# Optimization experiments

Hardware: AMD Instinct MI355X
Metric: run time of the kernel (lower is better)

## Reference

```python
import jax, jax.numpy as jnp
import numpy as np
import math

H = 12   # num_attention_heads
DH = 64  # attention_head_size
D = H * DH  # hidden_size = 768


def _split_heads(x):
    # [b, s, D] -> [b, H, s, DH]
    b, s, _ = x.shape
    return x.reshape(b, s, H, DH).transpose(0, 2, 1, 3)


def setup_inputs() -> dict:
    key = jax.random.key(0)
    ks = jax.random.split(key, 8)
    B, S, G, NUM_CTX = 32, 512, 16, 8
    real_b = B // NUM_CTX
    inp = {
        "hidden_states": jax.random.normal(ks[0], (B, S, D), dtype=jnp.float32),
        "attention_mask": jnp.zeros((B, 1, 1, S), dtype=jnp.float32),
        "global_tokens_embed": jax.random.normal(ks[1], (real_b, G, D), dtype=jnp.float32),
        "Wq": jax.random.normal(ks[2], (D, D), dtype=jnp.float32) * 0.02,
        "bq": jnp.zeros((D,), dtype=jnp.float32),
        "Wk": jax.random.normal(ks[3], (D, D), dtype=jnp.float32) * 0.02,
        "bk": jnp.zeros((D,), dtype=jnp.float32),
        "Wv": jax.random.normal(ks[4], (D, D), dtype=jnp.float32) * 0.02,
        "bv": jnp.zeros((D,), dtype=jnp.float32),
        "num_ctx": 8,
    }
    return inp


def reference(hidden_states, attention_mask, global_tokens_embed,
              Wq, bq, Wk, bk, Wv, bv, num_ctx):
    B, S, _ = hidden_states.shape
    real_b = B // num_ctx
    G = global_tokens_embed.shape[1]
    scale = 1.0 / math.sqrt(DH)

    # Q/K/V projections for packed contexts
    q = _split_heads(hidden_states @ Wq + bq)   # [B,H,S,DH]
    k = _split_heads(hidden_states @ Wk + bk)
    v = _split_heads(hidden_states @ Wv + bv)

    # Global token projections
    gq = _split_heads(global_tokens_embed @ Wq + bq)  # [real_b,H,G,DH]
    gk = _split_heads(global_tokens_embed @ Wk + bk)
    gv = _split_heads(global_tokens_embed @ Wv + bv)

    # ---- Global-token cross attention over all contexts of each real batch ----
    # [B,H,S,DH] -> [real_b, H, num_ctx*S, DH]
    full_k = k.transpose(0, 2, 1, 3).reshape(real_b, num_ctx * S, H, DH).transpose(0, 2, 1, 3)
    full_v = v.transpose(0, 2, 1, 3).reshape(real_b, num_ctx * S, H, DH).transpose(0, 2, 1, 3)
    full_k = jnp.concatenate([gk, full_k], axis=2)  # [real_b,H,G+num_ctx*S,DH]
    full_v = jnp.concatenate([gv, full_v], axis=2)

    g_scores = jnp.einsum('bhgd,bhkd->bhgk', gq, full_k) * scale
    g_mask = attention_mask.reshape(real_b, num_ctx * S)[:, None, None, :]
    g_mask = jnp.concatenate([jnp.zeros((real_b, 1, 1, G), g_mask.dtype), g_mask], axis=3)
    g_scores = g_scores + g_mask
    g_probs = jax.nn.softmax(g_scores, axis=-1)
    g_ctx = jnp.einsum('bhgk,bhkd->bhgd', g_probs, full_v)
    g_ctx = g_ctx.transpose(0, 2, 1, 3).reshape(real_b, G, D)  # [real_b,G,D]

    # ---- Local attention: each context attends to its own tokens + global tokens ----
    gk_rep = jnp.broadcast_to(gk[:, None], (real_b, num_ctx, H, G, DH)).reshape(B, H, G, DH)
    gv_rep = jnp.broadcast_to(gv[:, None], (real_b, num_ctx, H, G, DH)).reshape(B, H, G, DH)
    k2 = jnp.concatenate([gk_rep, k], axis=2)  # [B,H,G+S,DH]
    v2 = jnp.concatenate([gv_rep, v], axis=2)
    mask2 = jnp.concatenate([jnp.zeros((B, 1, 1, G), attention_mask.dtype), attention_mask], axis=3)

    scores = jnp.einsum('bhqd,bhkd->bhqk', q, k2) * scale + mask2  # [B,H,S,G+S]
    probs = jax.nn.softmax(scores, axis=-1)
    ctx = jnp.einsum('bhqk,bhkd->bhqd', probs, v2)
    ctx = ctx.transpose(0, 2, 1, 3).reshape(B, S, D)  # [B,S,D]

    return ctx, g_ctx
```

## Files before the change

kernel.cpp:

```cpp
#include <hip/hip_runtime.h>
#include <hip/hip_bf16.h>
#include <stdint.h>

#define NH 12
#define DHD 64
#define DM 768
#define BB 32
#define SS 512
#define GG 16
#define NCTX 8
#define RBATCH 4
#define OUTG_OFF ((size_t)BB * SS * DM)

#define XROWS 16512
#define NALL 2304
#define NX8 (XROWS * DM / 8)
#define NB8 (NALL / 8)
#define NM8 (BB * SS / 8)

#define LOG2E 1.4426950408889634f
#define QSCALE 0.18033688011112042f

typedef __bf16 bf16x8 __attribute__((ext_vector_type(8)));
typedef float f32x4 __attribute__((ext_vector_type(4)));
typedef float f32x16 __attribute__((ext_vector_type(16)));

__device__ __forceinline__ float b2f(unsigned short u) {
    union { unsigned int i; float f; } x;
    x.i = ((unsigned int)u) << 16;
    return x.f;
}
__device__ __forceinline__ unsigned short f2b(float f) {
    __hip_bfloat16 h = __float2bfloat16(f);
    return *reinterpret_cast<unsigned short*>(&h);
}
__device__ __forceinline__ unsigned int pk2(float a, float b) {
    return ((unsigned int)f2b(b) << 16) | (unsigned int)f2b(a);
}
__device__ __forceinline__ float ex2(float x) {
    return __builtin_amdgcn_exp2f(x);
}
__device__ __forceinline__ float ldv(const void* p, size_t i, int isf32) {
    return isf32 ? ((const float*)p)[i] : b2f(((const unsigned short*)p)[i]);
}
__device__ __forceinline__ void stv(void* p, size_t i, int isf32, float v) {
    if (isf32) ((float*)p)[i] = v;
    else       ((unsigned short*)p)[i] = f2b(v);
}
__device__ __forceinline__ void async_cp16(const unsigned short* g, unsigned short* l) {
    __builtin_amdgcn_global_load_lds(
        (const __attribute__((address_space(1))) unsigned int*)g,
        (__attribute__((address_space(3))) unsigned int*)l, 16, 0, 0);
}

__device__ __forceinline__ void vt_pair_store(unsigned int* Vt32, int vr, int scc,
                                              uint4 a, uint4 b, int ldq) {
    const unsigned int* au = (const unsigned int*)&a;
    const unsigned int* bu = (const unsigned int*)&b;
    #pragma unroll
    for (int i = 0; i < 4; i++) {
        const int d0 = scc + 2 * i;
        const int swz = ((vr >> 3) ^ ((d0 >> 3) & 7));
        const int i32 = d0 * ldq + (swz << 2) + ((vr & 7) >> 1);
        Vt32[i32]       = __builtin_amdgcn_perm(bu[i], au[i], 0x05040100u);
        Vt32[i32 + ldq] = __builtin_amdgcn_perm(bu[i], au[i], 0x07060302u);
    }
}

__global__ __launch_bounds__(256) void detect_dtype(
    const unsigned short* __restrict__ Wq, int* __restrict__ flag)
{
    __shared__ int hi, zz;
    if (threadIdx.x == 0) { hi = 0; zz = 0; }
    __syncthreads();
    int lh = 0, lz = 0;
    for (int i = threadIdx.x; i < 4096; i += 256) {
        unsigned short u = Wq[2 * i];
        if (((u >> 7) & 0xFF) >= 130) lh++;
        if (u == 0) lz++;
    }
    atomicAdd(&hi, lh);
    atomicAdd(&zz, lz);
    __syncthreads();
    if (threadIdx.x == 0) *flag = (hi > 512 || zz > 3500) ? 1 : 0;
}

__global__ __launch_bounds__(256) void cvt_x(
    const void* __restrict__ hs, const void* __restrict__ gte,
    const void* __restrict__ bq, const void* __restrict__ bk,
    const void* __restrict__ bv, const void* __restrict__ mask,
    const int* __restrict__ flag,
    unsigned short* __restrict__ Xb, unsigned short* __restrict__ b_all,
    unsigned short* __restrict__ wmask)
{
    const int e = blockIdx.x * 256 + threadIdx.x;
    const int isf32 = *flag;
    if (e < NX8) {
        const int base = e * 8;
        const int row = base / DM, col = base % DM;
        unsigned short o8[8];
        if (row < 16384) {
            if (isf32) {
                float4 a = ((const float4*)hs)[e * 2];
                float4 c = ((const float4*)hs)[e * 2 + 1];
                o8[0]=f2b(a.x); o8[1]=f2b(a.y); o8[2]=f2b(a.z); o8[3]=f2b(a.w);
                o8[4]=f2b(c.x); o8[5]=f2b(c.y); o8[6]=f2b(c.z); o8[7]=f2b(c.w);
            } else {
                *(uint4*)o8 = ((const uint4*)hs)[e];
            }
        } else if (row < 16448) {
            size_t soff = (size_t)(row - 16384) * DM + col;
            #pragma unroll
            for (int i = 0; i < 8; i++) o8[i] = f2b(ldv(gte, soff + i, isf32));
        } else {
            #pragma unroll
            for (int i = 0; i < 8; i++) o8[i] = 0;
        }
        *(uint4*)&Xb[base] = *(const uint4*)o8;
    } else if (e < NX8 + NB8) {
        const int i0 = (e - NX8) * 8;
        #pragma unroll
        for (int i = 0; i < 8; i++) {
            int ng = i0 + i;
            int z = ng / DM;
            const void* src = (z == 0) ? bq : (z == 1) ? bk : bv;
            b_all[ng] = f2b(ldv(src, ng % DM, isf32));
        }
    } else if (e < NX8 + NB8 + NM8) {
        const int i0 = (e - NX8 - NB8) * 8;
        #pragma unroll
        for (int i = 0; i < 8; i++)
            wmask[i0 + i] = f2b(ldv(mask, i0 + i, isf32) * LOG2E);
    }
}

__global__ __launch_bounds__(256) void cvt_w(
    const void* __restrict__ Wq, const void* __restrict__ Wk,
    const void* __restrict__ Wv, const int* __restrict__ flag,
    unsigned short* __restrict__ Wt)
{
    __shared__ float T[64][65];
    const int kt = blockIdx.x;
    const int ngt = blockIdx.y;
    const int z = ngt / 12, nt = ngt % 12;
    const int tid = threadIdx.x;
    const int isf32 = *flag;
    const void* W = (z == 0) ? Wq : (z == 1) ? Wk : Wv;

    for (int jj = 0; jj < 16; jj++) {
        int el = tid + jj * 256;
        int r = el >> 6, c = el & 63;
        T[r][c] = ldv(W, (size_t)(kt * 64 + r) * DM + nt * 64 + c, isf32);
    }
    __syncthreads();
    for (int jj = 0; jj < 16; jj++) {
        int el = tid + jj * 256;
        int rn = el >> 6, ck = el & 63;
        Wt[(size_t)(z * DM + nt * 64 + rn) * DM + kt * 64 + ck] = f2b(T[ck][rn]);
    }
}

#define QKV_NWG (129 * 18)
__global__ __launch_bounds__(256) void qkv_gemm(
    const unsigned short* __restrict__ Xb,
    const unsigned short* __restrict__ Wt,
    const unsigned short* __restrict__ b_all,
    unsigned short* __restrict__ q, unsigned short* __restrict__ kk_,
    unsigned short* __restrict__ v,
    unsigned short* __restrict__ gq, unsigned short* __restrict__ gk,
    unsigned short* __restrict__ gv)
{
    __shared__ __align__(16) unsigned short As[2][128 * 32];
    __shared__ __align__(16) unsigned short Bs[2][128 * 32];

    const int orig = blockIdx.x;
    const int q8 = QKV_NWG >> 3, r8 = QKV_NWG & 7;
    const int xcd = orig & 7, lin = orig >> 3;
    const int swz = (xcd < r8 ? xcd * (q8 + 1) : r8 * (q8 + 1) + (xcd - r8) * q8) + lin;
    const int mt = swz / 18, nt = swz - mt * 18;

    const int tid = threadIdx.x;
    const int wave = tid >> 6, lane = tid & 63;
    const int quad = lane >> 4, l16 = lane & 15;
    const int wm = wave & 1, wn = wave >> 1;
    const int z = nt / 6;
    unsigned short* YL = (z == 0) ? q : (z == 1) ? kk_ : v;
    unsigned short* YG = (z == 0) ? gq : (z == 1) ? gk : gv;
    const float qsc = (z == 0) ? QSCALE : 1.0f;

    const int sr = tid >> 2, sc = (tid & 3) * 8;

    const unsigned short* Arow0 = &Xb[(size_t)(mt * 128 + sr) * DM + sc];
    const unsigned short* Arow1 = Arow0 + (size_t)64 * DM;
    const unsigned short* Brow0 = &Wt[(size_t)(nt * 128 + sr) * DM + sc];
    const unsigned short* Brow1 = Brow0 + (size_t)64 * DM;

    f32x4 acc[4][4];
    #pragma unroll
    for (int i = 0; i < 4; i++)
        for (int j = 0; j < 4; j++)
            for (int r = 0; r < 4; r++) acc[i][j][r] = 0.f;

    async_cp16(Arow0, &As[0][wave * 512]);
    async_cp16(Arow1, &As[0][2048 + wave * 512]);
    async_cp16(Brow0, &Bs[0][wave * 512]);
    async_cp16(Brow1, &Bs[0][2048 + wave * 512]);
    __syncthreads();

    int cur = 0;
    for (int t = 0; t < 24; t++) {
        if (t < 23) {
            const int kn = (t + 1) * 32;
            async_cp16(Arow0 + kn, &As[cur ^ 1][wave * 512]);
            async_cp16(Arow1 + kn, &As[cur ^ 1][2048 + wave * 512]);
            async_cp16(Brow0 + kn, &Bs[cur ^ 1][wave * 512]);
            async_cp16(Brow1 + kn, &Bs[cur ^ 1][2048 + wave * 512]);
        }

        bf16x8 af[4], bf[4];
        #pragma unroll
        for (int ib = 0; ib < 4; ib++)
            af[ib] = *(const bf16x8*)&As[cur][(wm * 64 + ib * 16 + l16) * 32 + quad * 8];
        #pragma unroll
        for (int jb = 0; jb < 4; jb++)
            bf[jb] = *(const bf16x8*)&Bs[cur][(wn * 64 + jb * 16 + l16) * 32 + quad * 8];
        #pragma unroll
        for (int ib = 0; ib < 4; ib++)
            #pragma unroll
            for (int jb = 0; jb < 4; jb++)
                acc[ib][jb] = __builtin_amdgcn_mfma_f32_16x16x32_bf16(
                    bf[jb], af[ib], acc[ib][jb], 0, 0, 0);

        if (t < 23) __syncthreads();
        cur ^= 1;
    }

    #pragma unroll
    for (int ib = 0; ib < 4; ib++) {
        const int m = mt * 128 + wm * 64 + ib * 16 + l16;
        if (m >= 16448) continue;
        const bool loc = (m < 16384);
        const int b = m >> 9, s = m & 511;
        const int gl = m - 16384;
        const int rbx = gl >> 4, g = gl & 15;
        #pragma unroll
        for (int jb = 0; jb < 4; jb++) {
            const int ng0 = nt * 128 + wn * 64 + jb * 16 + quad * 4;
            const int o = ng0 - z * DM;
            const int h = o >> 6, dh0 = o & 63;
            const uint2 bu = *(const uint2*)&b_all[ng0];
            const unsigned short* bp = (const unsigned short*)&bu;
            const float y0 = (acc[ib][jb][0] + b2f(bp[0])) * qsc;
            const float y1 = (acc[ib][jb][1] + b2f(bp[1])) * qsc;
            const float y2 = (acc[ib][jb][2] + b2f(bp[2])) * qsc;
            const float y3 = (acc[ib][jb][3] + b2f(bp[3])) * qsc;
            uint2 o2;
            o2.x = pk2(y0, y1);
            o2.y = pk2(y2, y3);
            if (loc) {
                *(uint2*)&YL[(((size_t)b * NH + h) * SS + s) * DHD + dh0] = o2;
            } else {
                *(uint2*)&YG[(((size_t)rbx * NH + h) * GG + g) * DHD + dh0] = o2;
            }
        }
    }
}

#define AL_NWG (4 * NH * BB)
__global__ __launch_bounds__(256) void attn_local(
    const unsigned short* __restrict__ q,
    const unsigned short* __restrict__ k,
    const unsigned short* __restrict__ v,
    const unsigned short* __restrict__ gk,
    const unsigned short* __restrict__ gv,
    const unsigned short* __restrict__ wmask,
    const int* __restrict__ flag,
    void* __restrict__ out)
{
    __shared__ __align__(16) unsigned short Ks[64 * 64];
    __shared__ __align__(16) unsigned short Vt[64 * 64];

    const int orig = blockIdx.x;
    const int swz = (orig & 7) * (AL_NWG / 8) + (orig >> 3);
    const int qt = swz & 3;
    const int hb = swz >> 2;
    const int h = hb % NH, b = hb / NH;

    const int rb = b >> 3;
    const int tid = threadIdx.x, wave = tid >> 6, lane = tid & 63;
    const int l31 = lane & 31, h8 = lane >> 5;
    const int isf32 = *flag;
    const int q0 = qt * 128 + wave * 32;

    const size_t bh = (size_t)b * NH + h;
    const unsigned short* qp = q + bh * SS * DHD;
    const unsigned short* kp = k + bh * SS * DHD;
    const unsigned short* vp = v + bh * SS * DHD;
    const size_t gbh = (size_t)rb * NH + h;
    const unsigned short* gkp = gk + gbh * GG * DHD;
    const unsigned short* gvp = gv + gbh * GG * DHD;

    bf16x8 qf[4];
    #pragma unroll
    for (int kb = 0; kb < 4; kb++)
        qf[kb] = *(const bf16x8*)&qp[(size_t)(q0 + l31) * DHD + kb * 16 + h8 * 8];

    f32x16 oacc[2];
    #pragma unroll
    for (int mb = 0; mb < 2; mb++)
        #pragma unroll
        for (int j = 0; j < 16; j++) oacc[mb][j] = 0.f;
    float m_s = -1e30f, l_s = 0.f;

    const int sr = tid >> 3, scc = (tid & 7) * 8;
    const int vr = sr * 2;
    const int agc = (((lane & 7) ^ ((lane >> 3) & 7)) << 3);
    const int arow = 8 * wave + (lane >> 3);
    unsigned int* Vt32 = (unsigned int*)Vt;

    for (int t = 0; t < 9; t++) {
        __syncthreads();
        if (t == 0) {
            if (sr < 16) {
                uint4 kx = *(const uint4*)&gkp[sr * DHD + scc];
                *(uint4*)&Ks[sr * 64 + (((scc >> 3) ^ (sr & 7)) << 3)] = kx;
            } else {
                uint4 zz4 = {0, 0, 0, 0};
                *(uint4*)&Ks[sr * 64 + (((scc >> 3) ^ (sr & 7)) << 3)] = zz4;
            }
            uint4 va = {0, 0, 0, 0}, vb = {0, 0, 0, 0};
            if (sr < 8) {
                va = *(const uint4*)&gvp[vr * DHD + scc];
                vb = *(const uint4*)&gvp[(vr + 1) * DHD + scc];
            }
            vt_pair_store(Vt32, vr, scc, va, vb, 32);
        } else {
            const int ks0 = (t - 1) * 64;
            #pragma unroll
            for (int p = 0; p < 2; p++)
                async_cp16(&kp[(size_t)(ks0 + p * 32 + arow) * DHD + agc],
                           &Ks[p * 2048 + wave * 512]);
            uint4 va = *(const uint4*)&vp[(size_t)(ks0 + vr) * DHD + scc];
            uint4 vb = *(const uint4*)&vp[(size_t)(ks0 + vr + 1) * DHD + scc];
            vt_pair_store(Vt32, vr, scc, va, vb, 32);
        }
        __syncthreads();

        f32x16 scA, scB;
        #pragma unroll
        for (int kt = 0; kt < 2; kt++) {
            f32x16 cc;
            #pragma unroll
            for (int j = 0; j < 16; j++) cc[j] = 0.f;
            if (kt == 0 || t > 0) {
                #pragma unroll
                for (int kb = 0; kb < 4; kb++) {
                    const int key = kt * 32 + l31;
                    bf16x8 kf = *(const bf16x8*)&Ks[key * 64 + (((kb * 2 + h8) ^ (key & 7)) << 3)];
                    cc = __builtin_amdgcn_mfma_f32_32x32x16_bf16(kf, qf[kb], cc, 0, 0, 0);
                }
                if (t > 0) {
                    #pragma unroll
                    for (int rg = 0; rg < 4; rg++) {
                        uint2 mu = *(const uint2*)&wmask[b * SS + (t - 1) * 64 + kt * 32 + rg * 8 + 4 * h8];
                        const unsigned short* mp = (const unsigned short*)&mu;
                        #pragma unroll
                        for (int r = 0; r < 4; r++)
                            cc[rg * 4 + r] += b2f(mp[r]);
                    }
                } else {
                    #pragma unroll
                    for (int j = 8; j < 16; j++) cc[j] = -1e30f;
                }
            } else {
                #pragma unroll
                for (int j = 0; j < 16; j++) cc[j] = -1e30f;
            }
            if (kt == 0) scA = cc; else scB = cc;
        }

        float mx = -1e30f;
        #pragma unroll
        for (int j = 0; j < 16; j++) mx = fmaxf(mx, scA[j]);
        #pragma unroll
        for (int j = 0; j < 16; j++) mx = fmaxf(mx, scB[j]);
        mx = fmaxf(mx, __shfl_xor(mx, 32, 64));
        if (!__all(mx <= m_s)) {
            const float mn = fmaxf(m_s, mx);
            const float alpha = ex2(m_s - mn);
            m_s = mn;
            l_s *= alpha;
            #pragma unroll
            for (int mb = 0; mb < 2; mb++)
                #pragma unroll
                for (int j = 0; j < 16; j++) oacc[mb][j] *= alpha;
        }
        float rs = 0.f;
        #pragma unroll
        for (int j = 0; j < 16; j++) { float pw = ex2(scA[j] - m_s); scA[j] = pw; rs += pw; }
        #pragma unroll
        for (int j = 0; j < 16; j++) { float pw = ex2(scB[j] - m_s); scB[j] = pw; rs += pw; }
        rs += __shfl_xor(rs, 32, 64);
        l_s += rs;

        #pragma unroll
        for (int kt = 0; kt < 2; kt++) {
            unsigned int wA[4], wB[4];
            #pragma unroll
            for (int g = 0; g < 4; g++) {
                const float s0 = (kt == 0) ? scA[4 * g + 0] : scB[4 * g + 0];
                const float s1 = (kt == 0) ? scA[4 * g + 1] : scB[4 * g + 1];
                const float s2 = (kt == 0) ? scA[4 * g + 2] : scB[4 * g + 2];
                const float s3 = (kt == 0) ? scA[4 * g + 3] : scB[4 * g + 3];
                wA[g] = pk2(s0, s1);
                wB[g] = pk2(s2, s3);
            }
            #pragma unroll
            for (int kb = 0; kb < 2; kb++) {
                auto ra  = __builtin_amdgcn_permlane32_swap(wA[2 * kb], wA[2 * kb + 1], false, false);
                auto rbp = __builtin_amdgcn_permlane32_swap(wB[2 * kb], wB[2 * kb + 1], false, false);
                union { unsigned int u[4]; bf16x8 v8; } pfu;
                pfu.u[0] = (unsigned int)ra[0];
                pfu.u[1] = (unsigned int)rbp[0];
                pfu.u[2] = (unsigned int)ra[1];
                pfu.u[3] = (unsigned int)rbp[1];
                const int kb2 = kt * 2 + kb;
                #pragma unroll
                for (int mb = 0; mb < 2; mb++) {
                    const int d = mb * 32 + l31;
                    bf16x8 vf = *(const bf16x8*)&Vt[d * 64 + (((kb2 * 2 + h8) ^ ((d >> 3) & 7)) << 3)];
                    oacc[mb] = __builtin_amdgcn_mfma_f32_32x32x16_bf16(vf, pfu.v8, oacc[mb], 0, 0, 0);
                }
            }
        }
    }

    const float inv = 1.f / l_s;
    const int s = q0 + l31;
    #pragma unroll
    for (int mb = 0; mb < 2; mb++) {
        #pragma unroll
        for (int rg = 0; rg < 4; rg++) {
            const int d0 = mb * 32 + rg * 8 + 4 * h8;
            const size_t idx = ((size_t)b * SS + s) * DM + h * DHD + d0;
            if (isf32) {
                float4 o4;
                o4.x = oacc[mb][rg * 4 + 0] * inv;
                o4.y = oacc[mb][rg * 4 + 1] * inv;
                o4.z = oacc[mb][rg * 4 + 2] * inv;
                o4.w = oacc[mb][rg * 4 + 3] * inv;
                *(float4*)&((float*)out)[idx] = o4;
            } else {
                uint2 o2;
                o2.x = pk2(oacc[mb][rg * 4 + 0] * inv, oacc[mb][rg * 4 + 1] * inv);
                o2.y = pk2(oacc[mb][rg * 4 + 2] * inv, oacc[mb][rg * 4 + 3] * inv);
                *(uint2*)&((unsigned short*)out)[idx] = o2;
            }
        }
    }
}

__global__ __launch_bounds__(256) void attn_gsplit(
    const unsigned short* __restrict__ k,
    const unsigned short* __restrict__ v,
    const unsigned short* __restrict__ gq,
    const unsigned short* __restrict__ gk,
    const unsigned short* __restrict__ gv,
    const unsigned short* __restrict__ wmask,
    float* __restrict__ Opart, float* __restrict__ Mpart,
    float* __restrict__ Lpart)
{
    __shared__ __align__(16) unsigned short Ks[128 * 64];
    __shared__ __align__(16) unsigned short Vt[64 * 128];
    __shared__ __align__(16) unsigned short Ps[4 * 16 * 64];

    const int h = blockIdx.x, rb = blockIdx.y, sp = blockIdx.z;
    const int tid = threadIdx.x, wave = tid >> 6, lane = tid & 63;
    const int quad = lane >> 4, l16 = lane & 15;

    const size_t gbh = (size_t)rb * NH + h;
    const unsigned short* gqp = gq + gbh * GG * DHD;
    const unsigned short* gkp = gk + gbh * GG * DHD;
    const unsigned short* gvp = gv + gbh * GG * DHD;

    bf16x8 aq[2];
    aq[0] = *(const bf16x8*)&gqp[l16 * DHD + quad * 8];
    aq[1] = *(const bf16x8*)&gqp[l16 * DHD + 32 + quad * 8];

    f32x4 oacc[4];
    #pragma unroll
    for (int db = 0; db < 4; db++)
        for (int r = 0; r < 4; r++) oacc[db][r] = 0.f;
    float m_s = -1e30f, l_s = 0.f;

    const int sr = tid >> 3, scc = (tid & 7) * 8;
    const int vr = sr * 2;
    const int agc = (((lane & 7) ^ ((lane >> 3) & 7)) << 3);
    const int arow = 8 * wave + (lane >> 3);
    unsigned short* myP = &Ps[wave * 1024];
    unsigned int* Vt32 = (unsigned int*)Vt;

    const int nt = (sp == 0) ? 9 : 8;
    for (int ti = 0; ti < nt; ti++) {
        const bool gtile = (sp == 0 && ti == 0);
        int cb = 0, soff = 0;
        __syncthreads();
        if (gtile) {
            if (sr < 16) {
                uint4 kx = *(const uint4*)&gkp[sr * DHD + scc];
                *(uint4*)&Ks[sr * 64 + (((scc >> 3) ^ (sr & 7)) << 3)] = kx;
                uint4 va = {0, 0, 0, 0}, vb = {0, 0, 0, 0};
                if (sr < 8) {
                    va = *(const uint4*)&gvp[vr * DHD + scc];
                    vb = *(const uint4*)&gvp[(vr + 1) * DHD + scc];
                }
                vt_pair_store(Vt32, vr, scc, va, vb, 64);
            } else {
                uint4 zz4 = {0, 0, 0, 0};
                *(uint4*)&Ks[sr * 64 + (((scc >> 3) ^ (sr & 7)) << 3)] = zz4;
            }
        } else {
            const int kidx = sp * 1024 + (ti - ((sp == 0) ? 1 : 0)) * 128;
            cb = rb * NCTX + (kidx >> 9);
            soff = kidx & 511;
            const unsigned short* kp = k + ((size_t)cb * NH + h) * SS * DHD;
            const unsigned short* vp = v + ((size_t)cb * NH + h) * SS * DHD;
            #pragma unroll
            for (int p = 0; p < 4; p++)
                async_cp16(&kp[(size_t)(soff + p * 32 + arow) * DHD + agc],
                           &Ks[p * 2048 + wave * 512]);
            #pragma unroll
            for (int pp = 0; pp < 2; pp++) {
                const int vrr = vr + pp * 64;
                uint4 va = *(const uint4*)&vp[(size_t)(soff + vrr) * DHD + scc];
                uint4 vb = *(const uint4*)&vp[(size_t)(soff + vrr + 1) * DHD + scc];
                vt_pair_store(Vt32, vrr, scc, va, vb, 64);
            }
        }
        __syncthreads();

        if (gtile && wave != 0) continue;

        const int nbn = gtile ? 1 : 2;
        f32x4 c[2];
        for (int hh = 0; hh < nbn; hh++) {
            f32x4 cc = {0.f, 0.f, 0.f, 0.f};
            const int key = wave * 32 + hh * 16 + l16;
            #pragma unroll
            for (int kd = 0; kd < 2; kd++) {
                bf16x8 kf = *(const bf16x8*)&Ks[key * 64 + (((kd * 4 + quad) ^ (key & 7)) << 3)];
                cc = __builtin_amdgcn_mfma_f32_16x16x32_bf16(kf, aq[kd], cc, 0, 0, 0);
            }
            if (!gtile) {
                uint2 mu = *(const uint2*)&wmask[cb * SS + soff + wave * 32 + hh * 16 + quad * 4];
                const unsigned short* mp = (const unsigned short*)&mu;
                #pragma unroll
                for (int r = 0; r < 4; r++)
                    cc[r] += b2f(mp[r]);
            }
            c[hh] = cc;
        }

        float mx = -1e30f;
        for (int hh = 0; hh < nbn; hh++)
            #pragma unroll
            for (int r = 0; r < 4; r++) mx = fmaxf(mx, c[hh][r]);
        mx = fmaxf(mx, __shfl_xor(mx, 16, 64));
        mx = fmaxf(mx, __shfl_xor(mx, 32, 64));
        const float mn = fmaxf(m_s, mx);
        const float alpha = ex2(m_s - mn);
        m_s = mn;
        float rs = 0.f;
        for (int hh = 0; hh < nbn; hh++)
            #pragma unroll
            for (int r = 0; r < 4; r++) {
                float p = ex2(c[hh][r] - mn);
                c[hh][r] = p;
                rs += p;
            }
        rs += __shfl_xor(rs, 16, 64);
        rs += __shfl_xor(rs, 32, 64);
        l_s = l_s * alpha + rs;
        #pragma unroll
        for (int db = 0; db < 4; db++)
            for (int r = 0; r < 4; r++) oacc[db][r] *= alpha;

        for (int hh = 0; hh < nbn; hh++) {
            uint2 pw;
            pw.x = pk2(c[hh][0], c[hh][1]);
            pw.y = pk2(c[hh][2], c[hh][3]);
            const int cch = ((hh * 2 + (quad >> 1)) ^ (l16 & 7));
            *(uint2*)&myP[l16 * 64 + cch * 8 + (quad & 1) * 4] = pw;
        }
        if (nbn == 1) {
            uint2 zz2; zz2.x = 0; zz2.y = 0;
            const int cch = ((2 + (quad >> 1)) ^ (l16 & 7));
            *(uint2*)&myP[l16 * 64 + cch * 8 + (quad & 1) * 4] = zz2;
        }

        bf16x8 pf = *(const bf16x8*)&myP[l16 * 64 + ((quad ^ (l16 & 7)) << 3)];
        #pragma unroll
        for (int db = 0; db < 4; db++) {
            const int d = db * 16 + l16;
            const int kc = wave * 4 + quad;
            bf16x8 vf = *(const bf16x8*)&Vt[d * 128 + ((kc ^ ((d >> 3) & 7)) << 3)];
            oacc[db] = __builtin_amdgcn_mfma_f32_16x16x32_bf16(vf, pf, oacc[db], 0, 0, 0);
        }
    }

    __syncthreads();
    float* Om = (float*)Ks;
    float* Mw = (float*)Vt;
    float* Lw = Mw + 64;
    #pragma unroll
    for (int db = 0; db < 4; db++)
        for (int r = 0; r < 4; r++)
            Om[(wave * 16 + l16) * 64 + db * 16 + quad * 4 + r] = oacc[db][r];
    if (quad == 0) {
        Mw[wave * 16 + l16] = m_s;
        Lw[wave * 16 + l16] = l_s;
    }
    __syncthreads();

    const size_t pbase = ((size_t)(sp * RBATCH + rb) * NH + h) * 1024;
    for (int e = tid; e < 1024; e += 256) {
        const int qrow = e >> 6, d = e & 63;
        float M = fmaxf(fmaxf(Mw[qrow], Mw[16 + qrow]), fmaxf(Mw[32 + qrow], Mw[48 + qrow]));
        float acc = 0.f, L = 0.f;
        #pragma unroll
        for (int w = 0; w < 4; w++) {
            float scw = ex2(Mw[w * 16 + qrow] - M);
            acc += Om[(w * 16 + qrow) * 64 + d] * scw;
            L += Lw[w * 16 + qrow] * scw;
        }
        Opart[pbase + e] = acc;
        if (d == 0) {
            Mpart[((sp * RBATCH + rb) * NH + h) * 16 + qrow] = M;
            Lpart[((sp * RBATCH + rb) * NH + h) * 16 + qrow] = L;
        }
    }
}

__global__ __launch_bounds__(256) void attn_gmerge(
    const float* __restrict__ Opart, const float* __restrict__ Mpart,
    const float* __restrict__ Lpart, const int* __restrict__ flag,
    void* __restrict__ out)
{
    const int h = blockIdx.x, rb = blockIdx.y;
    const int tid = threadIdx.x;
    const int isf32 = *flag;
    for (int e = tid; e < 1024; e += 256) {
        const int qrow = e >> 6, d = e & 63;
        float M = -1e30f;
        #pragma unroll
        for (int sp = 0; sp < 4; sp++)
            M = fmaxf(M, Mpart[((sp * RBATCH + rb) * NH + h) * 16 + qrow]);
        float acc = 0.f, L = 0.f;
        #pragma unroll
        for (int sp = 0; sp < 4; sp++) {
            const size_t pb = ((size_t)(sp * RBATCH + rb) * NH + h);
            float scs = ex2(Mpart[pb * 16 + qrow] - M);
            acc += Opart[pb * 1024 + e] * scs;
            L += Lpart[pb * 16 + qrow] * scs;
        }
        stv(out, OUTG_OFF + ((size_t)rb * GG + qrow) * DM + h * DHD + d, isf32, acc / L);
    }
}

extern "C" void kernel_launch(void* const* d_in, const int* in_sizes, int n_in,
                              void* d_out, int out_size, void* d_ws, size_t ws_size,
                              hipStream_t stream) {
    const void* hs   = d_in[0];
    const void* mask = d_in[1];
    const void* gte  = d_in[2];
    const void* Wq   = d_in[3];
    const void* bq   = d_in[4];
    const void* Wk   = d_in[5];
    const void* bk   = d_in[6];
    const void* Wv   = d_in[7];
    const void* bv   = d_in[8];

    const size_t qkv_sz = (size_t)BB * NH * SS * DHD;
    const size_t g_sz   = (size_t)RBATCH * NH * GG * DHD;
    const size_t msk_sz = (size_t)BB * SS;
    const size_t x_sz   = (size_t)XROWS * DM;
    const size_t wt_sz  = (size_t)NALL * DM;
    const size_t ba_sz  = (size_t)NALL;
    const size_t need_hw = 3 * qkv_sz + 3 * g_sz + msk_sz + x_sz + wt_sz + ba_sz;
    if (ws_size < need_hw * 2 + 16) return;

    unsigned short* q     = (unsigned short*)d_ws;
    unsigned short* kk    = q + qkv_sz;
    unsigned short* vv    = kk + qkv_sz;
    unsigned short* gq    = vv + qkv_sz;
    unsigned short* gk    = gq + g_sz;
    unsigned short* gv    = gk + g_sz;
    unsigned short* wmask = gv + g_sz;
    unsigned short* Xb    = wmask + msk_sz;
    unsigned short* Wt    = Xb + x_sz;
    unsigned short* b_all = Wt + wt_sz;
    int* flag = (int*)(b_all + ba_sz);
    float* Opart = (float*)Xb;
    float* Mpart = Opart + 4 * RBATCH * NH * 1024;
    float* Lpart = Mpart + 4 * RBATCH * NH * 16;

    detect_dtype<<<1, 256, 0, stream>>>((const unsigned short*)Wq, flag);

    const int cvt_items = NX8 + NB8 + NM8;
    cvt_x<<<(cvt_items + 255) / 256, 256, 0, stream>>>(
        hs, gte, bq, bk, bv, mask, flag, Xb, b_all, wmask);
    cvt_w<<<dim3(12, 36), 256, 0, stream>>>(Wq, Wk, Wv, flag, Wt);

    qkv_gemm<<<dim3(QKV_NWG), 256, 0, stream>>>(Xb, Wt, b_all, q, kk, vv, gq, gk, gv);

    attn_local<<<dim3(AL_NWG), 256, 0, stream>>>(
        q, kk, vv, gk, gv, wmask, flag, d_out);
    attn_gsplit<<<dim3(NH, RBATCH, 4), 256, 0, stream>>>(
        kk, vv, gq, gk, gv, wmask, Opart, Mpart, Lpart);
    attn_gmerge<<<dim3(NH, RBATCH), 256, 0, stream>>>(
        Opart, Mpart, Lpart, flag, d_out);
}
```

Baseline: 345.1 us.

## Triple-buffer QKV GEMM shared-memory tiles with partial vmcnt waits

Converts the QKV projection GEMM main loop from double to triple buffering of the A/B shared-memory tiles. Loads are issued two K-steps ahead, and the barrier waits with s_waitcnt vmcnt(4), so only the older stage's loads must finish while the newest stay in flight. The loop is unrolled by three with macros so the buffer indices are compile-time constants. This raises LDS use per block from 32KB to 48KB, which may lower occupancy, and it depends on the async copies being counted by vmcnt in issue order.

```diff
diff --git a/kernel.cpp b/kernel.cpp
--- a/kernel.cpp
+++ b/kernel.cpp
@@ -170,8 +170,8 @@
     unsigned short* __restrict__ gq, unsigned short* __restrict__ gk,
     unsigned short* __restrict__ gv)
 {
-    __shared__ __align__(16) unsigned short As[2][128 * 32];
-    __shared__ __align__(16) unsigned short Bs[2][128 * 32];
+    __shared__ __align__(16) unsigned short As[3][128 * 32];
+    __shared__ __align__(16) unsigned short Bs[3][128 * 32];
 
     const int orig = blockIdx.x;
     const int q8 = QKV_NWG >> 3, r8 = QKV_NWG & 7;
@@ -201,39 +201,59 @@
         for (int j = 0; j < 4; j++)
             for (int r = 0; r < 4; r++) acc[i][j][r] = 0.f;
 
-    async_cp16(Arow0, &As[0][wave * 512]);
-    async_cp16(Arow1, &As[0][2048 + wave * 512]);
-    async_cp16(Brow0, &Bs[0][wave * 512]);
-    async_cp16(Brow1, &Bs[0][2048 + wave * 512]);
-    __syncthreads();
-
-    int cur = 0;
-    for (int t = 0; t < 24; t++) {
-        if (t < 23) {
-            const int kn = (t + 1) * 32;
-            async_cp16(Arow0 + kn, &As[cur ^ 1][wave * 512]);
-            async_cp16(Arow1 + kn, &As[cur ^ 1][2048 + wave * 512]);
-            async_cp16(Brow0 + kn, &Bs[cur ^ 1][wave * 512]);
-            async_cp16(Brow1 + kn, &Bs[cur ^ 1][2048 + wave * 512]);
-        }
-
-        bf16x8 af[4], bf[4];
-        #pragma unroll
-        for (int ib = 0; ib < 4; ib++)
-            af[ib] = *(const bf16x8*)&As[cur][(wm * 64 + ib * 16 + l16) * 32 + quad * 8];
-        #pragma unroll
-        for (int jb = 0; jb < 4; jb++)
-            bf[jb] = *(const bf16x8*)&Bs[cur][(wn * 64 + jb * 16 + l16) * 32 + quad * 8];
-        #pragma unroll
-        for (int ib = 0; ib < 4; ib++)
-            #pragma unroll
-            for (int jb = 0; jb < 4; jb++)
-                acc[ib][jb] = __builtin_amdgcn_mfma_f32_16x16x32_bf16(
-                    bf[jb], af[ib], acc[ib][jb], 0, 0, 0);
-
-        if (t < 23) __syncthreads();
-        cur ^= 1;
-    }
+#define QKV_STAGE(kn_, bb) do {                                         \
+        async_cp16(Arow0 + (kn_), &As[(bb)][wave * 512]);               \
+        async_cp16(Arow1 + (kn_), &As[(bb)][2048 + wave * 512]);        \
+        async_cp16(Brow0 + (kn_), &Bs[(bb)][wave * 512]);               \
+        async_cp16(Brow1 + (kn_), &Bs[(bb)][2048 + wave * 512]);        \
+    } while (0)
+
+#define QKV_COMPUTE(bb) do {                                                         \
+        bf16x8 af[4], bf[4];                                                         \
+        _Pragma("unroll")                                                            \
+        for (int ib = 0; ib < 4; ib++)                                               \
+            af[ib] = *(const bf16x8*)&As[(bb)][(wm * 64 + ib * 16 + l16) * 32 + quad * 8]; \
+        _Pragma("unroll")                                                            \
+        for (int jb = 0; jb < 4; jb++)                                               \
+            bf[jb] = *(const bf16x8*)&Bs[(bb)][(wn * 64 + jb * 16 + l16) * 32 + quad * 8]; \
+        _Pragma("unroll")                                                            \
+        for (int ib = 0; ib < 4; ib++)                                               \
+            _Pragma("unroll")                                                        \
+            for (int jb = 0; jb < 4; jb++)                                           \
+                acc[ib][jb] = __builtin_amdgcn_mfma_f32_16x16x32_bf16(               \
+                    bf[jb], af[ib], acc[ib][jb], 0, 0, 0);                           \
+    } while (0)
+
+#define QKV_SYNC4 asm volatile("s_waitcnt vmcnt(4)\n\ts_barrier" ::: "memory")
+#define QKV_SYNC0 asm volatile("s_waitcnt vmcnt(0)\n\ts_barrier" ::: "memory")
+
+    QKV_STAGE(0, 0);
+    QKV_STAGE(32, 1);
+    QKV_SYNC4;
+
+    for (int t0 = 0; t0 < 21; t0 += 3) {
+        const int kb = t0 * 32;
+        QKV_STAGE(kb + 64, 2);
+        QKV_COMPUTE(0);
+        QKV_SYNC4;
+        QKV_STAGE(kb + 96, 0);
+        QKV_COMPUTE(1);
+        QKV_SYNC4;
+        QKV_STAGE(kb + 128, 1);
+        QKV_COMPUTE(2);
+        QKV_SYNC4;
+    }
+    QKV_STAGE(23 * 32, 2);
+    QKV_COMPUTE(0);
+    QKV_SYNC4;
+    QKV_COMPUTE(1);
+    QKV_SYNC0;
+    QKV_COMPUTE(2);
+
+#undef QKV_STAGE
+#undef QKV_COMPUTE
+#undef QKV_SYNC4
+#undef QKV_SYNC0
 
     #pragma unroll
     for (int ib = 0; ib < 4; ib++) {
```

After: 339.8 us. No clear change (-1.5%).
